# Kernel optimization log

Measured on AMD Instinct MI355X. Metric: run time of the kernel, lower is better.

The kernel has to match this reference:

```python
import jax, jax.numpy as jnp
import numpy as np


def setup_inputs() -> dict:
    key = jax.random.key(0)
    k1, k2, k3, k4 = jax.random.split(key, 4)
    b, c, h, w = 16, 1024, 32, 32
    dim = h * w  # 1024
    x = jax.random.normal(k1, (b, c, h, w), dtype=jnp.float32)
    cond_img = jax.random.normal(k2, (b, c, h, w), dtype=jnp.float32)
    # torch nn.Linear weights: (out_features, in_features), y = x @ W.T
    Wq = jax.random.normal(k3, (dim, dim), dtype=jnp.float32) * (dim ** -0.5)
    Wkv = jax.random.normal(k4, (2 * dim, dim), dtype=jnp.float32) * (dim ** -0.5)
    return {"x": x, "cond_img": cond_img, "Wq": Wq, "Wkv": Wkv}


def reference(x, cond_img, Wq, Wkv):
    b, c, h, w = x.shape
    dim = h * w
    scale = dim ** -0.5
    xf = x.reshape(b, c, dim)          # (b, c, dim)
    cf = cond_img.reshape(b, c, dim)   # (b, c, dim)
    q = jnp.einsum('bcd,od->bco', xf, Wq)          # (b, c, dim)
    kv = jnp.einsum('bcd,od->bco', cf, Wkv)        # (b, c, 2*dim)
    k, v = jnp.split(kv, 2, axis=-1)               # each (b, c, dim)
    attn = jnp.einsum('bic,bjc->bij', q, k) * scale  # (b, c, c)
    attn = jax.nn.softmax(attn, axis=-1)
    out = jnp.einsum('bij,bjc->bic', attn, v)      # (b, c, dim)
    return out.reshape(b, c, h, w)
```

## Files before the change

### kernel.cpp

```cpp
#include <hip/hip_runtime.h>
#include <stdint.h>


typedef __bf16 bf16_t;
typedef bf16_t bf16x8 __attribute__((ext_vector_type(8)));
typedef float f32x4 __attribute__((ext_vector_type(4)));

#define AS1 __attribute__((address_space(1)))
#define AS3 __attribute__((address_space(3)))

__device__ __forceinline__ uint16_t f2bf(float f) {
  bf16_t h = (bf16_t)f;
  return __builtin_bit_cast(uint16_t, h);
}

__global__ __launch_bounds__(256) void cvt_bf16(const float* __restrict__ in,
                                                uint16_t* __restrict__ out, int n4) {
  int i = blockIdx.x * 256 + threadIdx.x;
  if (i >= n4) return;
  float4 v = ((const float4*)in)[i];
  ushort4 o;
  o.x = f2bf(v.x); o.y = f2bf(v.y); o.z = f2bf(v.z); o.w = f2bf(v.w);
  ((ushort4*)out)[i] = o;
}

__device__ __forceinline__ void stage_half(const uint16_t* __restrict__ g, int ld,
                                           uint8_t* lds, int tid) {
#pragma unroll
  for (int i = 0; i < 2; ++i) {
    int c = i * 512 + tid;
    int row = c >> 3;
    int ch = c & 7;
    int sch = ch ^ (row & 7);
    const uint16_t* gp = g + row * ld + sch * 8;
    __builtin_amdgcn_global_load_lds((AS1 void*)gp, (AS3 void*)(lds + c * 16),
                                     16, 0, 0);
  }
}

template <int MODE>
__global__ __launch_bounds__(512, 2) void gemm_bt(
    const uint16_t* __restrict__ A, const uint16_t* __restrict__ B,
    void* __restrict__ C0, void* __restrict__ C1, int K, int N,
    long long sA, long long sB, long long sC, float scale) {
  __shared__ uint16_t As[2][2][8192];
  __shared__ uint16_t Bs[2][2][8192];

  const int tid = threadIdx.x;
  const int lane = tid & 63;
  const int wid = tid >> 6;
  const int wr = wid >> 2;
  const int wc = wid & 3;
  const int lr = lane & 15, lg = lane >> 4;
  const int ch0 = lr & 7;

  const int row0 = blockIdx.y * 256;
  const int col0 = blockIdx.x * 256;
  const int bz = blockIdx.z;
  const uint16_t* At = A + (long long)bz * sA + (long long)row0 * K;
  const uint16_t* Bt = B + (long long)bz * sB + (long long)col0 * K;

  const int NT = K >> 6;

  stage_half(At, K, (uint8_t*)&As[0][0][0], tid);
  stage_half(At + 128 * K, K, (uint8_t*)&As[0][1][0], tid);
  stage_half(Bt, K, (uint8_t*)&Bs[0][0][0], tid);
  stage_half(Bt + 128 * K, K, (uint8_t*)&Bs[0][1][0], tid);
  if (NT > 1) {
    stage_half(At + 64, K, (uint8_t*)&As[1][0][0], tid);
    stage_half(At + 128 * K + 64, K, (uint8_t*)&As[1][1][0], tid);
    asm volatile("s_waitcnt vmcnt(4)" ::: "memory");
  } else {
    asm volatile("s_waitcnt vmcnt(0)" ::: "memory");
  }
  asm volatile("s_barrier" ::: "memory");

  f32x4 acc[8][4] = {};

  for (int t = 0; t < NT; ++t) {
    const int buf = t & 1;
    bf16x8 fa[8][2];
    const uint8_t* abase = (const uint8_t*)&As[buf][wr][0];
#pragma unroll
    for (int mi = 0; mi < 8; ++mi) {
      const int rr = mi * 16 + lr;
#pragma unroll
      for (int kk = 0; kk < 2; ++kk)
        fa[mi][kk] =
            *(const bf16x8*)(abase + rr * 128 + (((kk * 4 + lg) ^ ch0) << 4));
    }
    const uint8_t* bbase = (const uint8_t*)&Bs[buf][wc >> 1][0];
#pragma unroll
    for (int ni = 0; ni < 4; ++ni) {
      const int rb = (wc & 1) * 64 + ni * 16 + lr;
      bf16x8 fb[2];
#pragma unroll
      for (int kk = 0; kk < 2; ++kk)
        fb[kk] =
            *(const bf16x8*)(bbase + rb * 128 + (((kk * 4 + lg) ^ ch0) << 4));
      if (ni == 0 && t + 1 < NT)
        stage_half(Bt + (t + 1) * 64, K, (uint8_t*)&Bs[buf ^ 1][0][0], tid);
      if (ni == 1 && t + 1 < NT)
        stage_half(Bt + 128 * K + (t + 1) * 64, K, (uint8_t*)&Bs[buf ^ 1][1][0],
                   tid);
      if (ni == 2 && t + 2 < NT)
        stage_half(At + (t + 2) * 64, K, (uint8_t*)&As[buf][0][0], tid);
      if (ni == 3 && t + 2 < NT)
        stage_half(At + 128 * K + (t + 2) * 64, K, (uint8_t*)&As[buf][1][0],
                   tid);
      asm volatile("s_barrier" ::: "memory");
      __builtin_amdgcn_s_setprio(1);
#pragma unroll
      for (int kk = 0; kk < 2; ++kk)
#pragma unroll
        for (int mi = 0; mi < 8; ++mi)
          acc[mi][ni] = __builtin_amdgcn_mfma_f32_16x16x32_bf16(
              fa[mi][kk], fb[kk], acc[mi][ni], 0, 0, 0);
      __builtin_amdgcn_s_setprio(0);
      if (ni == 3) {
        if (t + 2 < NT)
          asm volatile("s_waitcnt vmcnt(4)" ::: "memory");
        else
          asm volatile("s_waitcnt vmcnt(0)" ::: "memory");
      }
      asm volatile("s_barrier" ::: "memory");
    }
  }

#pragma unroll
  for (int mi = 0; mi < 8; ++mi) {
#pragma unroll
    for (int ni = 0; ni < 4; ++ni) {
      const int row = row0 + wr * 128 + mi * 16 + lg * 4;
      const int col = col0 + wc * 64 + ni * 16 + lr;
      if (MODE == 0) {
        uint16_t* C = (uint16_t*)C0;
#pragma unroll
        for (int j = 0; j < 4; ++j)
          C[(long long)(row + j) * N + col] = f2bf(acc[mi][ni][j]);
      } else if (MODE == 1) {
        if (col < 1024) {
          uint16_t* Kp = (uint16_t*)C0;
#pragma unroll
          for (int j = 0; j < 4; ++j)
            Kp[(long long)(row + j) * 1024 + col] = f2bf(acc[mi][ni][j]);
        } else {
          const int b = row >> 10, jj = row & 1023;
          ushort4 o;
          o.x = f2bf(acc[mi][ni][0]);
          o.y = f2bf(acc[mi][ni][1]);
          o.z = f2bf(acc[mi][ni][2]);
          o.w = f2bf(acc[mi][ni][3]);
          uint16_t* Vp = (uint16_t*)C1;
          *(ushort4*)(Vp + (long long)b * 1048576 +
                      (long long)(col - 1024) * 1024 + jj) = o;
        }
      } else {
        float* C = (float*)C0;
#pragma unroll
        for (int j = 0; j < 4; ++j)
          C[(long long)bz * sC + (long long)(row + j) * N + col] =
              acc[mi][ni][j] * scale;
      }
    }
  }
}

__global__ __launch_bounds__(256) void softmax_rows(const float* __restrict__ S,
                                                    uint16_t* __restrict__ P) {
  const int row = blockIdx.x;
  const int t = threadIdx.x;
  const int w = t >> 6, l = t & 63;
  __shared__ float red[8];

  const float4 v = ((const float4*)(S + (long long)row * 1024))[t];
  float m = fmaxf(fmaxf(v.x, v.y), fmaxf(v.z, v.w));
#pragma unroll
  for (int o = 1; o < 64; o <<= 1) m = fmaxf(m, __shfl_xor(m, o, 64));
  if (l == 0) red[w] = m;
  __syncthreads();
  m = fmaxf(fmaxf(red[0], red[1]), fmaxf(red[2], red[3]));

  float e0 = __expf(v.x - m), e1 = __expf(v.y - m);
  float e2 = __expf(v.z - m), e3 = __expf(v.w - m);
  float s = e0 + e1 + e2 + e3;
#pragma unroll
  for (int o = 1; o < 64; o <<= 1) s += __shfl_xor(s, o, 64);
  if (l == 0) red[4 + w] = s;
  __syncthreads();
  s = red[4] + red[5] + red[6] + red[7];
  const float inv = 1.0f / s;

  ushort4 o4;
  o4.x = f2bf(e0 * inv); o4.y = f2bf(e1 * inv);
  o4.z = f2bf(e2 * inv); o4.w = f2bf(e3 * inv);
  ((ushort4*)P)[(long long)row * 256 + t] = o4;
}

extern "C" void kernel_launch(void* const* d_in, const int* in_sizes, int n_in,
                              void* d_out, int out_size, void* d_ws, size_t ws_size,
                              hipStream_t stream) {
  const float* x    = (const float*)d_in[0];
  const float* cond = (const float*)d_in[1];
  const float* Wq   = (const float*)d_in[2];
  const float* Wkv  = (const float*)d_in[3];
  float* out = (float*)d_out;

  uint8_t* ws = (uint8_t*)d_ws;
  const long long MiB = 1ll << 20;
  uint16_t* XB   = (uint16_t*)(ws + 0 * MiB);
  uint16_t* CB   = (uint16_t*)(ws + 32 * MiB);
  float*    S    = (float*)(ws + 0 * MiB);
  uint16_t* WQB  = (uint16_t*)(ws + 64 * MiB);
  uint16_t* WKVB = (uint16_t*)(ws + 66 * MiB);
  uint16_t* Q    = (uint16_t*)(ws + 70 * MiB);
  uint16_t* Kb   = (uint16_t*)(ws + 102 * MiB);
  uint16_t* VT   = (uint16_t*)(ws + 134 * MiB);

  cvt_bf16<<<16384, 256, 0, stream>>>(x, XB, 16777216 / 4);
  cvt_bf16<<<16384, 256, 0, stream>>>(cond, CB, 16777216 / 4);
  cvt_bf16<<<1024, 256, 0, stream>>>(Wq, WQB, 1048576 / 4);
  cvt_bf16<<<2048, 256, 0, stream>>>(Wkv, WKVB, 2097152 / 4);

  gemm_bt<0><<<dim3(4, 64, 1), 512, 0, stream>>>(XB, WQB, Q, nullptr, 1024,
                                                 1024, 0, 0, 0, 1.0f);
  gemm_bt<1><<<dim3(8, 64, 1), 512, 0, stream>>>(CB, WKVB, Kb, VT, 1024, 2048,
                                                 0, 0, 0, 1.0f);
  gemm_bt<2><<<dim3(4, 4, 16), 512, 0, stream>>>(Q, Kb, S, nullptr, 1024, 1024,
                                                 1048576, 1048576, 1048576,
                                                 0.03125f);
  softmax_rows<<<16384, 256, 0, stream>>>(S, Q);
  gemm_bt<2><<<dim3(4, 4, 16), 512, 0, stream>>>(Q, VT, out, nullptr, 1024,
                                                 1024, 1048576, 1048576,
                                                 1048576, 1.0f);
}
```

Measured before the change: 269.2 us.

## Restructure GEMM main loop into 8-phase 2x2 quadrant schedule with workgroup swizzle

The GEMM inner loop is rewritten as a two-K-tile unrolled sequence of eight phases. Each phase loads a 4x2 quadrant of A/B fragments from LDS, issues one global-to-LDS stage, and runs 16 MFMAs behind barriers and an explicit lgkmcnt wait. This cuts register pressure from the full 8-row A fragment set and spreads prefetches more evenly across the loop. A workgroup-ID swizzle also remaps blocks, interleaving groups of eight to improve L2 locality across the chiplets. The risks are the extra barriers per tile and the loop's assumption that the tile count is even.

Result: faster. 256.9 us (-4.6%).

```diff
diff --git a/kernel.cpp b/kernel.cpp
--- a/kernel.cpp
+++ b/kernel.cpp
@@ -38,6 +38,38 @@
   }
 }
 
+#define PH(AB, BB, H, N2, DO_A, DO_B, STAGE, VMW)                              \
+  {                                                                            \
+    if (DO_A) {                                                                \
+      _Pragma("unroll") for (int mi = 0; mi < 4; ++mi)                         \
+          _Pragma("unroll") for (int kk = 0; kk < 2; ++kk)                     \
+              aF[mi][kk] = *(const bf16x8*)((AB) + ((H)*64 + mi*16 + lr)*128 + \
+                                            (((kk*4 + lg) ^ ch0) << 4));       \
+    }                                                                          \
+    if (DO_B) {                                                                \
+      _Pragma("unroll") for (int nj = 0; nj < 2; ++nj)                         \
+          _Pragma("unroll") for (int kk = 0; kk < 2; ++kk)                     \
+              bAll[(N2)*2 + nj][kk] = *(const bf16x8*)(                        \
+                  (BB) + ((wc & 1)*64 + ((N2)*2 + nj)*16 + lr)*128 +           \
+                  (((kk*4 + lg) ^ ch0) << 4));                                 \
+    }                                                                          \
+    STAGE;                                                                     \
+    asm volatile("s_barrier" ::: "memory");                                    \
+    asm volatile("s_waitcnt lgkmcnt(0)" ::: "memory");                         \
+    __builtin_amdgcn_sched_barrier(0);                                         \
+    __builtin_amdgcn_s_setprio(1);                                             \
+    _Pragma("unroll") for (int kk = 0; kk < 2; ++kk)                           \
+        _Pragma("unroll") for (int mi = 0; mi < 4; ++mi)                       \
+            _Pragma("unroll") for (int nj = 0; nj < 2; ++nj)                   \
+                acc[(H)*4 + mi][(N2)*2 + nj] =                                 \
+                    __builtin_amdgcn_mfma_f32_16x16x32_bf16(                   \
+                        aF[mi][kk], bAll[(N2)*2 + nj][kk],                     \
+                        acc[(H)*4 + mi][(N2)*2 + nj], 0, 0, 0);                \
+    __builtin_amdgcn_s_setprio(0);                                             \
+    VMW;                                                                       \
+    asm volatile("s_barrier" ::: "memory");                                    \
+  }
+
 template <int MODE>
 __global__ __launch_bounds__(512, 2) void gemm_bt(
     const uint16_t* __restrict__ A, const uint16_t* __restrict__ B,
@@ -54,77 +86,67 @@
   const int lr = lane & 15, lg = lane >> 4;
   const int ch0 = lr & 7;
 
-  const int row0 = blockIdx.y * 256;
-  const int col0 = blockIdx.x * 256;
-  const int bz = blockIdx.z;
+  const int gx = gridDim.x, gy = gridDim.y;
+  const int nwg = gx * gy * gridDim.z;
+  int fid = blockIdx.x + gx * (blockIdx.y + gy * blockIdx.z);
+  int swz = (fid & 7) * (nwg >> 3) + (fid >> 3);
+  const int bx = swz % gx;
+  const int rem = swz / gx;
+  const int by = rem % gy;
+  const int bz = rem / gy;
+
+  const int row0 = by * 256;
+  const int col0 = bx * 256;
   const uint16_t* At = A + (long long)bz * sA + (long long)row0 * K;
   const uint16_t* Bt = B + (long long)bz * sB + (long long)col0 * K;
 
   const int NT = K >> 6;
-
+  const int NIT = NT >> 1;
+
+  stage_half(Bt, K, (uint8_t*)&Bs[0][0][0], tid);
+  stage_half(Bt + 128 * K, K, (uint8_t*)&Bs[0][1][0], tid);
   stage_half(At, K, (uint8_t*)&As[0][0][0], tid);
   stage_half(At + 128 * K, K, (uint8_t*)&As[0][1][0], tid);
-  stage_half(Bt, K, (uint8_t*)&Bs[0][0][0], tid);
-  stage_half(Bt + 128 * K, K, (uint8_t*)&Bs[0][1][0], tid);
-  if (NT > 1) {
-    stage_half(At + 64, K, (uint8_t*)&As[1][0][0], tid);
-    stage_half(At + 128 * K + 64, K, (uint8_t*)&As[1][1][0], tid);
-    asm volatile("s_waitcnt vmcnt(4)" ::: "memory");
-  } else {
-    asm volatile("s_waitcnt vmcnt(0)" ::: "memory");
-  }
+  stage_half(Bt + 64, K, (uint8_t*)&Bs[1][0][0], tid);
+  stage_half(Bt + 128 * K + 64, K, (uint8_t*)&Bs[1][1][0], tid);
+  asm volatile("s_waitcnt vmcnt(4)" ::: "memory");
   asm volatile("s_barrier" ::: "memory");
 
   f32x4 acc[8][4] = {};
-
-  for (int t = 0; t < NT; ++t) {
-    const int buf = t & 1;
-    bf16x8 fa[8][2];
-    const uint8_t* abase = (const uint8_t*)&As[buf][wr][0];
-#pragma unroll
-    for (int mi = 0; mi < 8; ++mi) {
-      const int rr = mi * 16 + lr;
-#pragma unroll
-      for (int kk = 0; kk < 2; ++kk)
-        fa[mi][kk] =
-            *(const bf16x8*)(abase + rr * 128 + (((kk * 4 + lg) ^ ch0) << 4));
-    }
-    const uint8_t* bbase = (const uint8_t*)&Bs[buf][wc >> 1][0];
-#pragma unroll
-    for (int ni = 0; ni < 4; ++ni) {
-      const int rb = (wc & 1) * 64 + ni * 16 + lr;
-      bf16x8 fb[2];
-#pragma unroll
-      for (int kk = 0; kk < 2; ++kk)
-        fb[kk] =
-            *(const bf16x8*)(bbase + rb * 128 + (((kk * 4 + lg) ^ ch0) << 4));
-      if (ni == 0 && t + 1 < NT)
-        stage_half(Bt + (t + 1) * 64, K, (uint8_t*)&Bs[buf ^ 1][0][0], tid);
-      if (ni == 1 && t + 1 < NT)
-        stage_half(Bt + 128 * K + (t + 1) * 64, K, (uint8_t*)&Bs[buf ^ 1][1][0],
-                   tid);
-      if (ni == 2 && t + 2 < NT)
-        stage_half(At + (t + 2) * 64, K, (uint8_t*)&As[buf][0][0], tid);
-      if (ni == 3 && t + 2 < NT)
-        stage_half(At + 128 * K + (t + 2) * 64, K, (uint8_t*)&As[buf][1][0],
-                   tid);
-      asm volatile("s_barrier" ::: "memory");
-      __builtin_amdgcn_s_setprio(1);
-#pragma unroll
-      for (int kk = 0; kk < 2; ++kk)
-#pragma unroll
-        for (int mi = 0; mi < 8; ++mi)
-          acc[mi][ni] = __builtin_amdgcn_mfma_f32_16x16x32_bf16(
-              fa[mi][kk], fb[kk], acc[mi][ni], 0, 0, 0);
-      __builtin_amdgcn_s_setprio(0);
-      if (ni == 3) {
-        if (t + 2 < NT)
-          asm volatile("s_waitcnt vmcnt(4)" ::: "memory");
-        else
-          asm volatile("s_waitcnt vmcnt(0)" ::: "memory");
-      }
-      asm volatile("s_barrier" ::: "memory");
-    }
+  bf16x8 aF[4][2];
+  bf16x8 bAll[4][2];
+
+  for (int i = 0; i < NIT; ++i) {
+    const int t1 = 2 * i + 1;
+    const int tn0 = 2 * i + 2, tn1 = 2 * i + 3;
+    const uint8_t* a0 = (const uint8_t*)&As[0][wr][0];
+    const uint8_t* a1 = (const uint8_t*)&As[1][wr][0];
+    const uint8_t* b0 = (const uint8_t*)&Bs[0][wc >> 1][0];
+    const uint8_t* b1 = (const uint8_t*)&Bs[1][wc >> 1][0];
+
+    PH(a0, b0, 0, 0, true, true,
+       stage_half(At + t1 * 64, K, (uint8_t*)&As[1][0][0], tid), );
+    PH(a0, b0, 0, 1, false, true,
+       stage_half(At + 128 * K + t1 * 64, K, (uint8_t*)&As[1][1][0], tid), );
+    PH(a0, b0, 1, 0, true, false,
+       if (tn0 < NT) stage_half(Bt + tn0 * 64, K, (uint8_t*)&Bs[0][0][0], tid), );
+    PH(a0, b0, 1, 1, false, false,
+       if (tn0 < NT) stage_half(Bt + 128 * K + tn0 * 64, K,
+                                (uint8_t*)&Bs[0][1][0], tid),
+       if (i + 1 < NIT) asm volatile("s_waitcnt vmcnt(4)" ::: "memory");
+       else asm volatile("s_waitcnt vmcnt(0)" ::: "memory"));
+    PH(a1, b1, 0, 0, true, true,
+       if (tn0 < NT) stage_half(At + tn0 * 64, K, (uint8_t*)&As[0][0][0], tid), );
+    PH(a1, b1, 0, 1, false, true,
+       if (tn0 < NT) stage_half(At + 128 * K + tn0 * 64, K,
+                                (uint8_t*)&As[0][1][0], tid), );
+    PH(a1, b1, 1, 0, true, false,
+       if (tn1 < NT) stage_half(Bt + tn1 * 64, K, (uint8_t*)&Bs[1][0][0], tid), );
+    PH(a1, b1, 1, 1, false, false,
+       if (tn1 < NT) stage_half(Bt + 128 * K + tn1 * 64, K,
+                                (uint8_t*)&Bs[1][1][0], tid),
+       if (i + 1 < NIT) asm volatile("s_waitcnt vmcnt(4)" ::: "memory");
+       else asm volatile("s_waitcnt vmcnt(0)" ::: "memory"));
   }
 
 #pragma unroll
```

## Switch GEMM to 4-stage K32 LDS pipeline with workgroup swizzle

Applied to the files above, without the earlier changes.

Reduces the K tile from 64 to 32 and uses a four-buffer LDS ring with three tiles prefetched ahead, with an XOR swizzle adapted to 64-byte rows. It remaps workgroup IDs so consecutive blocks are spread across groups for cache locality. The goal is to hide global-load latency better and improve L2 reuse, at the cost of more barriers per unit of MFMA work.

After: 263.0 us. 2.3% less time.

```diff
diff --git a/kernel.cpp b/kernel.cpp
--- a/kernel.cpp
+++ b/kernel.cpp
@@ -24,17 +24,18 @@
   ((ushort4*)out)[i] = o;
 }
 
-__device__ __forceinline__ void stage_half(const uint16_t* __restrict__ g, int ld,
-                                           uint8_t* lds, int tid) {
+__device__ __forceinline__ void stage32(const uint16_t* __restrict__ g, int ldK,
+                                        uint16_t* lds, int tid) {
 #pragma unroll
   for (int i = 0; i < 2; ++i) {
     int c = i * 512 + tid;
-    int row = c >> 3;
-    int ch = c & 7;
-    int sch = ch ^ (row & 7);
-    const uint16_t* gp = g + row * ld + sch * 8;
-    __builtin_amdgcn_global_load_lds((AS1 void*)gp, (AS3 void*)(lds + c * 16),
-                                     16, 0, 0);
+    int row = c >> 2;
+    int ch = c & 3;
+    int sch = ch ^ ((row >> 1) & 3);
+    const uint16_t* gp = g + row * ldK + sch * 8;
+    __builtin_amdgcn_global_load_lds((AS1 void*)gp,
+                                     (AS3 void*)((uint8_t*)lds + c * 16), 16, 0,
+                                     0);
   }
 }
 
@@ -43,8 +44,8 @@
     const uint16_t* __restrict__ A, const uint16_t* __restrict__ B,
     void* __restrict__ C0, void* __restrict__ C1, int K, int N,
     long long sA, long long sB, long long sC, float scale) {
-  __shared__ uint16_t As[2][2][8192];
-  __shared__ uint16_t Bs[2][2][8192];
+  __shared__ uint16_t As[4][8192];
+  __shared__ uint16_t Bs[4][8192];
 
   const int tid = threadIdx.x;
   const int lane = tid & 63;
@@ -52,79 +53,85 @@
   const int wr = wid >> 2;
   const int wc = wid & 3;
   const int lr = lane & 15, lg = lane >> 4;
-  const int ch0 = lr & 7;
-
-  const int row0 = blockIdx.y * 256;
-  const int col0 = blockIdx.x * 256;
-  const int bz = blockIdx.z;
+  const int chnk = ((lg ^ ((lr >> 1) & 3)) << 4);
+
+  const int gx = gridDim.x, gy = gridDim.y;
+  const int nwg = gx * gy * gridDim.z;
+  int fid = blockIdx.x + gx * (blockIdx.y + gy * blockIdx.z);
+  int swz = (fid & 7) * (nwg >> 3) + (fid >> 3);
+  const int bx = swz % gx;
+  const int rem = swz / gx;
+  const int by = rem % gy;
+  const int bz = rem / gy;
+
+  const int row0 = by * 256;
+  const int col0 = bx * 256;
   const uint16_t* At = A + (long long)bz * sA + (long long)row0 * K;
   const uint16_t* Bt = B + (long long)bz * sB + (long long)col0 * K;
 
-  const int NT = K >> 6;
-
-  stage_half(At, K, (uint8_t*)&As[0][0][0], tid);
-  stage_half(At + 128 * K, K, (uint8_t*)&As[0][1][0], tid);
-  stage_half(Bt, K, (uint8_t*)&Bs[0][0][0], tid);
-  stage_half(Bt + 128 * K, K, (uint8_t*)&Bs[0][1][0], tid);
-  if (NT > 1) {
-    stage_half(At + 64, K, (uint8_t*)&As[1][0][0], tid);
-    stage_half(At + 128 * K + 64, K, (uint8_t*)&As[1][1][0], tid);
-    asm volatile("s_waitcnt vmcnt(4)" ::: "memory");
-  } else {
-    asm volatile("s_waitcnt vmcnt(0)" ::: "memory");
-  }
-  asm volatile("s_barrier" ::: "memory");
+  const int NT = K >> 5;
+
+  stage32(At, K, &As[0][0], tid);
+  stage32(Bt, K, &Bs[0][0], tid);
+  stage32(At + 32, K, &As[1][0], tid);
+  stage32(Bt + 32, K, &Bs[1][0], tid);
+  stage32(At + 64, K, &As[2][0], tid);
+  stage32(Bt + 64, K, &Bs[2][0], tid);
+  asm volatile("s_waitcnt vmcnt(8)" ::: "memory");
+  __builtin_amdgcn_s_barrier();
 
   f32x4 acc[8][4] = {};
 
   for (int t = 0; t < NT; ++t) {
-    const int buf = t & 1;
-    bf16x8 fa[8][2];
-    const uint8_t* abase = (const uint8_t*)&As[buf][wr][0];
+    const uint16_t* sa = &As[t & 3][0];
+    const uint16_t* sb = &Bs[t & 3][0];
+    const int tp = t + 3;
+
+    bf16x8 fa[8], fb0, fb1;
+#pragma unroll
+    for (int mi = 0; mi < 8; ++mi)
+      fa[mi] = *(const bf16x8*)((const uint8_t*)sa +
+                                (wr * 128 + mi * 16 + lr) * 64 + chnk);
+    fb0 = *(const bf16x8*)((const uint8_t*)sb + (wc * 64 + 0 * 16 + lr) * 64 +
+                           chnk);
+    fb1 = *(const bf16x8*)((const uint8_t*)sb + (wc * 64 + 1 * 16 + lr) * 64 +
+                           chnk);
+    if (tp < NT) stage32(At + tp * 32, K, &As[tp & 3][0], tid);
+    __builtin_amdgcn_s_barrier();
+    __builtin_amdgcn_s_setprio(1);
 #pragma unroll
     for (int mi = 0; mi < 8; ++mi) {
-      const int rr = mi * 16 + lr;
-#pragma unroll
-      for (int kk = 0; kk < 2; ++kk)
-        fa[mi][kk] =
-            *(const bf16x8*)(abase + rr * 128 + (((kk * 4 + lg) ^ ch0) << 4));
+      acc[mi][0] = __builtin_amdgcn_mfma_f32_16x16x32_bf16(fa[mi], fb0,
+                                                           acc[mi][0], 0, 0, 0);
+      acc[mi][1] = __builtin_amdgcn_mfma_f32_16x16x32_bf16(fa[mi], fb1,
+                                                           acc[mi][1], 0, 0, 0);
     }
-    const uint8_t* bbase = (const uint8_t*)&Bs[buf][wc >> 1][0];
-#pragma unroll
-    for (int ni = 0; ni < 4; ++ni) {
-      const int rb = (wc & 1) * 64 + ni * 16 + lr;
-      bf16x8 fb[2];
-#pragma unroll
-      for (int kk = 0; kk < 2; ++kk)
-        fb[kk] =
-            *(const bf16x8*)(bbase + rb * 128 + (((kk * 4 + lg) ^ ch0) << 4));
-      if (ni == 0 && t + 1 < NT)
-        stage_half(Bt + (t + 1) * 64, K, (uint8_t*)&Bs[buf ^ 1][0][0], tid);
-      if (ni == 1 && t + 1 < NT)
-        stage_half(Bt + 128 * K + (t + 1) * 64, K, (uint8_t*)&Bs[buf ^ 1][1][0],
-                   tid);
-      if (ni == 2 && t + 2 < NT)
-        stage_half(At + (t + 2) * 64, K, (uint8_t*)&As[buf][0][0], tid);
-      if (ni == 3 && t + 2 < NT)
-        stage_half(At + 128 * K + (t + 2) * 64, K, (uint8_t*)&As[buf][1][0],
-                   tid);
-      asm volatile("s_barrier" ::: "memory");
-      __builtin_amdgcn_s_setprio(1);
-#pragma unroll
-      for (int kk = 0; kk < 2; ++kk)
-#pragma unroll
-        for (int mi = 0; mi < 8; ++mi)
-          acc[mi][ni] = __builtin_amdgcn_mfma_f32_16x16x32_bf16(
-              fa[mi][kk], fb[kk], acc[mi][ni], 0, 0, 0);
-      __builtin_amdgcn_s_setprio(0);
-      if (ni == 3) {
-        if (t + 2 < NT)
-          asm volatile("s_waitcnt vmcnt(4)" ::: "memory");
-        else
-          asm volatile("s_waitcnt vmcnt(0)" ::: "memory");
-      }
-      asm volatile("s_barrier" ::: "memory");
+    __builtin_amdgcn_s_setprio(0);
+    __builtin_amdgcn_s_barrier();
+
+    bf16x8 fb2, fb3;
+    fb2 = *(const bf16x8*)((const uint8_t*)sb + (wc * 64 + 2 * 16 + lr) * 64 +
+                           chnk);
+    fb3 = *(const bf16x8*)((const uint8_t*)sb + (wc * 64 + 3 * 16 + lr) * 64 +
+                           chnk);
+    if (tp < NT) stage32(Bt + tp * 32, K, &Bs[tp & 3][0], tid);
+    __builtin_amdgcn_s_barrier();
+    __builtin_amdgcn_s_setprio(1);
+#pragma unroll
+    for (int mi = 0; mi < 8; ++mi) {
+      acc[mi][2] = __builtin_amdgcn_mfma_f32_16x16x32_bf16(fa[mi], fb2,
+                                                           acc[mi][2], 0, 0, 0);
+      acc[mi][3] = __builtin_amdgcn_mfma_f32_16x16x32_bf16(fa[mi], fb3,
+                                                           acc[mi][3], 0, 0, 0);
     }
+    __builtin_amdgcn_s_setprio(0);
+    if (t + 3 < NT)
+      asm volatile("s_waitcnt vmcnt(8)" ::: "memory");
+    else if (t + 2 < NT)
+      asm volatile("s_waitcnt vmcnt(4)" ::: "memory");
+    else if (t + 1 < NT)
+      asm volatile("s_waitcnt vmcnt(0)" ::: "memory");
+    __builtin_amdgcn_s_barrier();
   }
 
 #pragma unroll
```
